# Performance work log

Measured on AMD Instinct MI355X. Metric: run time of the kernel, lower is better.

## Reference

```python
import jax, jax.numpy as jnp
import numpy as np

B, N, M, D = 4, 512, 512, 128
H, DOUT = 256, 128

def setup_inputs() -> dict:
    key = jax.random.key(0)
    k = jax.random.split(key, 4)
    X = jax.random.normal(k[0], (B, N, D), dtype=jnp.float32)
    Y = jax.random.normal(k[1], (B, M, D), dtype=jnp.float32)
    W1 = jax.random.normal(k[2], (2 * D, H), dtype=jnp.float32) / np.sqrt(2 * D)
    b1 = jnp.zeros((H,), dtype=jnp.float32)
    W2 = jax.random.normal(k[3], (H, DOUT), dtype=jnp.float32) / np.sqrt(H)
    b2 = jnp.zeros((DOUT,), dtype=jnp.float32)
    return {"X": X, "Y": Y, "W1": W1, "b1": b1, "W2": W2, "b2": b2}

def reference(X, Y, W1, b1, W2, b2):
    # pairs[b,n,m,:] = concat(Y[b,m], X[b,n])  -> [B,N,M,2D]
    n_ = X.shape[1]
    m_ = Y.shape[1]
    Ye = jnp.broadcast_to(Y[:, None, :, :], (X.shape[0], n_, m_, Y.shape[-1]))
    Xe = jnp.broadcast_to(X[:, :, None, :], (X.shape[0], n_, m_, X.shape[-1]))
    pairs = jnp.concatenate([Ye, Xe], axis=-1)
    # pointwise MLP: Linear -> ReLU -> Linear
    hdn = jax.nn.relu(jnp.einsum('bnmd,dh->bnmh', pairs, W1) + b1)
    Z = jnp.einsum('bnmh,ho->bnmo', hdn, W2) + b2
    # pool='sum' over the M (neighbor) dimension
    return jnp.sum(Z, axis=2)  # [B, N, DOUT]
```

## Files before the change

### kernel.cpp

```cpp
#include <hip/hip_runtime.h>

#define BB    4
#define NN    512
#define MM    512
#define DD    128
#define HH    256
#define DOUTC 128

typedef float v2f __attribute__((ext_vector_type(2)));
typedef float v4f __attribute__((ext_vector_type(4)));

__global__ __launch_bounds__(1024) void precompute_ac(
    const float* __restrict__ X, const float* __restrict__ Y,
    const float* __restrict__ W1, const float* __restrict__ b1,
    float* __restrict__ AC)
{
    __shared__ __align__(16) float rows[16][DD];
    __shared__ __align__(16) v4f mrg[3][4][4][64];
    const int bid = blockIdx.x;
    const int t   = threadIdx.x;
    const int isC = bid >> 7;
    const int r0  = (bid & 127) * 16;
    const float* src = isC ? X : Y;

    if (t < 512)
        reinterpret_cast<v4f*>(&rows[0][0])[t] =
            reinterpret_cast<const v4f*>(src + (size_t)r0 * DD)[t];
    __syncthreads();

    const int hq = t & 63;
    const int dq = (t >> 6) & 3;
    const int rs = t >> 8;
    const int d0 = dq * 32;
    const float* wp = W1 + (isC ? DD * HH : 0) + hq * 4;

    v4f acc[4];
#pragma unroll
    for (int r = 0; r < 4; ++r) acc[r] = (v4f){0.f, 0.f, 0.f, 0.f};

#pragma unroll 2
    for (int dg = 0; dg < 32; dg += 4) {
        const int d = d0 + dg;
        const v4f w0 = *reinterpret_cast<const v4f*>(&wp[(d + 0) * HH]);
        const v4f w1 = *reinterpret_cast<const v4f*>(&wp[(d + 1) * HH]);
        const v4f w2 = *reinterpret_cast<const v4f*>(&wp[(d + 2) * HH]);
        const v4f w3 = *reinterpret_cast<const v4f*>(&wp[(d + 3) * HH]);
#pragma unroll
        for (int r = 0; r < 4; ++r) {
            const v4f rv = *reinterpret_cast<const v4f*>(&rows[rs * 4 + r][d]);
            acc[r] += w0 * rv.x;
            acc[r] += w1 * rv.y;
            acc[r] += w2 * rv.z;
            acc[r] += w3 * rv.w;
        }
    }

    if (dq > 0) {
#pragma unroll
        for (int r = 0; r < 4; ++r) mrg[dq - 1][rs][r][hq] = acc[r];
    }
    __syncthreads();
    if (dq == 0) {
#pragma unroll
        for (int r = 0; r < 4; ++r) {
#pragma unroll
            for (int p = 0; p < 3; ++p) acc[r] += mrg[p][rs][r][hq];
        }
        v4f bias = (v4f){0.f, 0.f, 0.f, 0.f};
        if (isC) bias = *reinterpret_cast<const v4f*>(&b1[hq * 4]);
#pragma unroll
        for (int r = 0; r < 4; ++r)
            *reinterpret_cast<v4f*>(
                &AC[((size_t)(isC * 2048 + r0 + rs * 4 + r)) * HH + hq * 4]) =
                acc[r] + bias;
    }
}

__global__ __launch_bounds__(512) void fused_main(
    const float* __restrict__ A, const float* __restrict__ C,
    const float* __restrict__ W2, const float* __restrict__ b2,
    float* __restrict__ out)
{
    __shared__ __align__(16) v4f mergeA[8][4][64];
    __shared__ __align__(16) v4f mergeS[8][64];
    __shared__ __align__(16) float S[4][HH];
    const int bid = blockIdx.x;
    const int b   = bid >> 7;
    const int n0  = (bid & 127) * 4;
    const int t   = threadIdx.x;
    const int l   = t & 63;
    const int qm  = t >> 6;
    const int h0  = l * 4;

    const float* Cb = C + ((size_t)(b * NN + n0)) * HH + h0;
    v4f c4[4];
#pragma unroll
    for (int j = 0; j < 4; ++j)
        c4[j] = *reinterpret_cast<const v4f*>(&Cb[(size_t)j * HH]);
    v2f c01[4], c23[4];
#pragma unroll
    for (int j = 0; j < 4; ++j) {
        c01[j] = (v2f){c4[j].x, c4[j].y};
        c23[j] = (v2f){c4[j].z, c4[j].w};
    }

    float acc[4][4];
#pragma unroll
    for (int j = 0; j < 4; ++j)
#pragma unroll
        for (int u = 0; u < 4; ++u) acc[j][u] = 0.f;
    v2f sat01 = (v2f){0.f, 0.f}, sat23 = (v2f){0.f, 0.f};

    const float* Ab = A + ((size_t)(b * MM + qm * 64)) * HH + h0;
#pragma unroll 4
    for (int m = 0; m < 64; ++m) {
        const v4f a = *reinterpret_cast<const v4f*>(&Ab[(size_t)m * HH]);
        const v2f a01 = (v2f){a.x, a.y};
        const v2f a23 = (v2f){a.z, a.w};
        sat01 += a01;
        sat23 += a23;
#pragma unroll
        for (int j = 0; j < 4; ++j) {
            const v2f s01 = a01 + c01[j];
            const v2f s23 = a23 + c23[j];
            acc[j][0] += fabsf(s01.x);
            acc[j][1] += fabsf(s01.y);
            acc[j][2] += fabsf(s23.x);
            acc[j][3] += fabsf(s23.y);
        }
    }

#pragma unroll
    for (int j = 0; j < 4; ++j)
        mergeA[qm][j][l] = (v4f){acc[j][0], acc[j][1], acc[j][2], acc[j][3]};
    mergeS[qm][l] = (v4f){sat01.x, sat01.y, sat23.x, sat23.y};
    __syncthreads();

    if (qm < 4) {
        const int r = qm;
        v4f sum = mergeA[0][r][l];
#pragma unroll
        for (int p = 1; p < 8; ++p) sum += mergeA[p][r][l];
        v4f st = mergeS[0][l];
#pragma unroll
        for (int p = 1; p < 8; ++p) st += mergeS[p][l];
        const v4f sval = 0.5f * (st + 512.f * c4[r] + sum);
        *reinterpret_cast<v4f*>(&S[r][h0]) = sval;
    }
    __syncthreads();

    const int o0 = (t & 31) * 4;
    const int r  = (t >> 5) & 3;
    const int kq = t >> 7;
    const int k0 = kq * 64;
    v4f a4 = (v4f){0.f, 0.f, 0.f, 0.f};
    const float* w2p = W2 + o0;
#pragma unroll 4
    for (int k = k0; k < k0 + 64; k += 4) {
        const v4f sv = *reinterpret_cast<const v4f*>(&S[r][k]);
        const v4f wA = *reinterpret_cast<const v4f*>(&w2p[(k + 0) * DOUTC]);
        const v4f wB = *reinterpret_cast<const v4f*>(&w2p[(k + 1) * DOUTC]);
        const v4f wC = *reinterpret_cast<const v4f*>(&w2p[(k + 2) * DOUTC]);
        const v4f wD = *reinterpret_cast<const v4f*>(&w2p[(k + 3) * DOUTC]);
        a4 += wA * sv.x;
        a4 += wB * sv.y;
        a4 += wC * sv.z;
        a4 += wD * sv.w;
    }
    v4f* red = reinterpret_cast<v4f*>(&mergeA[0][0][0]);
    if (kq) red[(kq - 1) * 128 + (t & 127)] = a4;
    __syncthreads();
    if (kq == 0) {
#pragma unroll
        for (int p = 0; p < 3; ++p) a4 += red[p * 128 + (t & 127)];
        a4 += 512.f * (*reinterpret_cast<const v4f*>(&b2[o0]));
        *reinterpret_cast<v4f*>(&out[((size_t)(b * NN + n0 + r)) * DOUTC + o0]) = a4;
    }
}

extern "C" void kernel_launch(void* const* d_in, const int* in_sizes, int n_in,
                              void* d_out, int out_size, void* d_ws, size_t ws_size,
                              hipStream_t stream) {
    const float* X  = (const float*)d_in[0];
    const float* Y  = (const float*)d_in[1];
    const float* W1 = (const float*)d_in[2];
    const float* b1 = (const float*)d_in[3];
    const float* W2 = (const float*)d_in[4];
    const float* b2 = (const float*)d_in[5];
    float* out = (float*)d_out;

    float* AC = (float*)d_ws;
    float* A  = AC;
    float* Cm = AC + 2048 * HH;

    hipLaunchKernelGGL(precompute_ac, dim3(256), dim3(1024), 0, stream,
                       X, Y, W1, b1, AC);
    hipLaunchKernelGGL(fused_main, dim3(512), dim3(512), 0, stream,
                       A, Cm, W2, b2, out);
}
```

Before: 42.29 us.

## Replace O(N·M) ReLU sum with per-feature sort, prefix sums and binary search

The sum over M of relu(a_m + c_n) is now computed per hidden feature by sorting the A column with a bitonic sort in shared memory, building a prefix sum, and binary-searching each c_n to get the count and sum of terms above the threshold. This replaces the O(N·M·H) brute-force accumulation with O((N+M)·log M·H) work. Precompute now writes A and C transposed into workspace, and a separate epilogue kernel does the W2 projection. The cost is one extra kernel launch, many __syncthreads rounds in the sort and scan, and strided transposed stores in the precompute kernel.

```diff
diff --git a/kernel.cpp b/kernel.cpp
--- a/kernel.cpp
+++ b/kernel.cpp
@@ -7,13 +7,12 @@
 #define HH    256
 #define DOUTC 128
 
-typedef float v2f __attribute__((ext_vector_type(2)));
 typedef float v4f __attribute__((ext_vector_type(4)));
 
 __global__ __launch_bounds__(1024) void precompute_ac(
     const float* __restrict__ X, const float* __restrict__ Y,
     const float* __restrict__ W1, const float* __restrict__ b1,
-    float* __restrict__ AC)
+    float* __restrict__ AT, float* __restrict__ CT)
 {
     __shared__ __align__(16) float rows[16][DD];
     __shared__ __align__(16) v4f mrg[3][4][4][64];
@@ -69,84 +68,117 @@
         v4f bias = (v4f){0.f, 0.f, 0.f, 0.f};
         if (isC) bias = *reinterpret_cast<const v4f*>(&b1[hq * 4]);
 #pragma unroll
-        for (int r = 0; r < 4; ++r)
+        for (int r = 0; r < 4; ++r) acc[r] += bias;
+
+        const int grow = r0 + rs * 4;
+        const int bb   = grow >> 9;
+        const int mm   = grow & 511;
+        float* Tb = isC ? CT : AT;
+#pragma unroll
+        for (int u = 0; u < 4; ++u) {
+            const v4f w = (v4f){acc[0][u], acc[1][u], acc[2][u], acc[3][u]};
             *reinterpret_cast<v4f*>(
-                &AC[((size_t)(isC * 2048 + r0 + rs * 4 + r)) * HH + hq * 4]) =
-                acc[r] + bias;
-    }
-}
-
-__global__ __launch_bounds__(512) void fused_main(
-    const float* __restrict__ A, const float* __restrict__ C,
-    const float* __restrict__ W2, const float* __restrict__ b2,
-    float* __restrict__ out)
+                &Tb[((size_t)(bb * HH + hq * 4 + u)) * 512 + mm]) = w;
+        }
+    }
+}
+
+__global__ __launch_bounds__(512) void sort_query(
+    const float* __restrict__ AT, const float* __restrict__ CT,
+    float* __restrict__ S)
 {
-    __shared__ __align__(16) v4f mergeA[8][4][64];
-    __shared__ __align__(16) v4f mergeS[8][64];
-    __shared__ __align__(16) float S[4][HH];
+    __shared__ float col[4][512];
+    __shared__ float t1[4][512];
+    __shared__ float t2[4][512];
     const int bid = blockIdx.x;
-    const int b   = bid >> 7;
-    const int n0  = (bid & 127) * 4;
+    const int b   = bid >> 6;
+    const int h0  = (bid & 63) * 4;
     const int t   = threadIdx.x;
-    const int l   = t & 63;
-    const int qm  = t >> 6;
-    const int h0  = l * 4;
-
-    const float* Cb = C + ((size_t)(b * NN + n0)) * HH + h0;
-    v4f c4[4];
-#pragma unroll
-    for (int j = 0; j < 4; ++j)
-        c4[j] = *reinterpret_cast<const v4f*>(&Cb[(size_t)j * HH]);
-    v2f c01[4], c23[4];
-#pragma unroll
-    for (int j = 0; j < 4; ++j) {
-        c01[j] = (v2f){c4[j].x, c4[j].y};
-        c23[j] = (v2f){c4[j].z, c4[j].w};
-    }
-
-    float acc[4][4];
-#pragma unroll
-    for (int j = 0; j < 4; ++j)
-#pragma unroll
-        for (int u = 0; u < 4; ++u) acc[j][u] = 0.f;
-    v2f sat01 = (v2f){0.f, 0.f}, sat23 = (v2f){0.f, 0.f};
-
-    const float* Ab = A + ((size_t)(b * MM + qm * 64)) * HH + h0;
-#pragma unroll 4
-    for (int m = 0; m < 64; ++m) {
-        const v4f a = *reinterpret_cast<const v4f*>(&Ab[(size_t)m * HH]);
-        const v2f a01 = (v2f){a.x, a.y};
-        const v2f a23 = (v2f){a.z, a.w};
-        sat01 += a01;
-        sat23 += a23;
-#pragma unroll
-        for (int j = 0; j < 4; ++j) {
-            const v2f s01 = a01 + c01[j];
-            const v2f s23 = a23 + c23[j];
-            acc[j][0] += fabsf(s01.x);
-            acc[j][1] += fabsf(s01.y);
-            acc[j][2] += fabsf(s23.x);
-            acc[j][3] += fabsf(s23.y);
-        }
-    }
-
-#pragma unroll
-    for (int j = 0; j < 4; ++j)
-        mergeA[qm][j][l] = (v4f){acc[j][0], acc[j][1], acc[j][2], acc[j][3]};
-    mergeS[qm][l] = (v4f){sat01.x, sat01.y, sat23.x, sat23.y};
-    __syncthreads();
-
-    if (qm < 4) {
-        const int r = qm;
-        v4f sum = mergeA[0][r][l];
-#pragma unroll
-        for (int p = 1; p < 8; ++p) sum += mergeA[p][r][l];
-        v4f st = mergeS[0][l];
-#pragma unroll
-        for (int p = 1; p < 8; ++p) st += mergeS[p][l];
-        const v4f sval = 0.5f * (st + 512.f * c4[r] + sum);
-        *reinterpret_cast<v4f*>(&S[r][h0]) = sval;
-    }
+
+    const float* Abase = AT + ((size_t)(b * HH + h0)) * 512;
+#pragma unroll
+    for (int u = 0; u < 4; ++u)
+        col[u][t] = Abase[(size_t)u * 512 + t];
+    __syncthreads();
+
+    for (int k = 2; k <= 512; k <<= 1) {
+        for (int j = k >> 1; j > 0; j >>= 1) {
+            const int p = t ^ j;
+            if (p > t) {
+                const bool asc = ((t & k) == 0);
+#pragma unroll
+                for (int u = 0; u < 4; ++u) {
+                    const float x = col[u][t];
+                    const float y = col[u][p];
+                    if ((x > y) == asc) { col[u][t] = y; col[u][p] = x; }
+                }
+            }
+            __syncthreads();
+        }
+    }
+
+#pragma unroll
+    for (int u = 0; u < 4; ++u)
+        t1[u][t] = col[u][t] + ((t >= 1) ? col[u][t - 1] : 0.f);
+    __syncthreads();
+    {
+        int d = 2;
+#pragma unroll
+        for (int s = 0; s < 8; ++s) {
+            if ((s & 1) == 0) {
+#pragma unroll
+                for (int u = 0; u < 4; ++u)
+                    t2[u][t] = t1[u][t] + ((t >= d) ? t1[u][t - d] : 0.f);
+            } else {
+#pragma unroll
+                for (int u = 0; u < 4; ++u)
+                    t1[u][t] = t2[u][t] + ((t >= d) ? t2[u][t - d] : 0.f);
+            }
+            __syncthreads();
+            d <<= 1;
+        }
+    }
+
+    const float* Cbase = CT + ((size_t)(b * HH + h0)) * 512;
+    float cv[4], negc[4];
+    int kk[4];
+#pragma unroll
+    for (int u = 0; u < 4; ++u) {
+        cv[u]   = Cbase[(size_t)u * 512 + t];
+        negc[u] = -cv[u];
+        kk[u]   = 0;
+    }
+#pragma unroll
+    for (int step = 512; step > 0; step >>= 1) {
+#pragma unroll
+        for (int u = 0; u < 4; ++u) {
+            const int nk = kk[u] + step;
+            if (nk <= 512 && col[u][nk - 1] < negc[u]) kk[u] = nk;
+        }
+    }
+
+    v4f s4;
+#pragma unroll
+    for (int u = 0; u < 4; ++u) {
+        const float T  = t1[u][511];
+        const float Pk = (kk[u] > 0) ? t1[u][kk[u] - 1] : 0.f;
+        s4[u] = (T - Pk) + (float)(512 - kk[u]) * cv[u];
+    }
+    *reinterpret_cast<v4f*>(&S[((size_t)(b * NN + t)) * HH + h0]) = s4;
+}
+
+__global__ __launch_bounds__(512) void epilogue(
+    const float* __restrict__ S, const float* __restrict__ W2,
+    const float* __restrict__ b2, float* __restrict__ out)
+{
+    __shared__ __align__(16) float Sl[4][HH];
+    __shared__ __align__(16) v4f red[3 * 128];
+    const int bn0 = blockIdx.x * 4;
+    const int t   = threadIdx.x;
+
+    if (t < 256)
+        reinterpret_cast<v4f*>(&Sl[0][0])[t] =
+            reinterpret_cast<const v4f*>(&S[(size_t)bn0 * HH])[t];
     __syncthreads();
 
     const int o0 = (t & 31) * 4;
@@ -157,7 +189,7 @@
     const float* w2p = W2 + o0;
 #pragma unroll 4
     for (int k = k0; k < k0 + 64; k += 4) {
-        const v4f sv = *reinterpret_cast<const v4f*>(&S[r][k]);
+        const v4f sv = *reinterpret_cast<const v4f*>(&Sl[r][k]);
         const v4f wA = *reinterpret_cast<const v4f*>(&w2p[(k + 0) * DOUTC]);
         const v4f wB = *reinterpret_cast<const v4f*>(&w2p[(k + 1) * DOUTC]);
         const v4f wC = *reinterpret_cast<const v4f*>(&w2p[(k + 2) * DOUTC]);
@@ -167,14 +199,13 @@
         a4 += wC * sv.z;
         a4 += wD * sv.w;
     }
-    v4f* red = reinterpret_cast<v4f*>(&mergeA[0][0][0]);
     if (kq) red[(kq - 1) * 128 + (t & 127)] = a4;
     __syncthreads();
     if (kq == 0) {
 #pragma unroll
         for (int p = 0; p < 3; ++p) a4 += red[p * 128 + (t & 127)];
         a4 += 512.f * (*reinterpret_cast<const v4f*>(&b2[o0]));
-        *reinterpret_cast<v4f*>(&out[((size_t)(b * NN + n0 + r)) * DOUTC + o0]) = a4;
+        *reinterpret_cast<v4f*>(&out[(size_t)(bn0 + r) * DOUTC + o0]) = a4;
     }
 }
 
@@ -189,12 +220,14 @@
     const float* b2 = (const float*)d_in[5];
     float* out = (float*)d_out;
 
-    float* AC = (float*)d_ws;
-    float* A  = AC;
-    float* Cm = AC + 2048 * HH;
+    float* AT = (float*)d_ws;
+    float* CT = AT + (size_t)BB * HH * 512;
+    float* S  = CT + (size_t)BB * HH * 512;
 
     hipLaunchKernelGGL(precompute_ac, dim3(256), dim3(1024), 0, stream,
-                       X, Y, W1, b1, AC);
-    hipLaunchKernelGGL(fused_main, dim3(512), dim3(512), 0, stream,
-                       A, Cm, W2, b2, out);
-}
+                       X, Y, W1, b1, AT, CT);
+    hipLaunchKernelGGL(sort_query, dim3(256), dim3(512), 0, stream,
+                       AT, CT, S);
+    hipLaunchKernelGGL(epilogue, dim3(BB * NN / 4), dim3(512), 0, stream,
+                       S, W2, b2, out);
+}
```

Result: slower. 45.01 us (+6.4%).

## Split abs-sum stage into M-chunked kernel, precompute A-column sums, add epilogue

Applied to the files above, without the earlier changes.

The abs-sum kernel now gives each block 8 n-rows and a quarter of the M dimension, so every loaded A row is reused across 8 C rows, and 1024 smaller blocks are launched. The sum of A over m (SAT) is no longer accumulated inside the hot loop. Two extra blocks in the precompute kernel compute it as colsum(Y)·W1. A new epilogue kernel reduces the partial sums and applies W2. This cuts per-element load work and raises parallelism, at the cost of a third launch and a workspace round trip for the partials.

```diff
diff --git a/kernel.cpp b/kernel.cpp
--- a/kernel.cpp
+++ b/kernel.cpp
@@ -13,114 +13,136 @@
 __global__ __launch_bounds__(1024) void precompute_ac(
     const float* __restrict__ X, const float* __restrict__ Y,
     const float* __restrict__ W1, const float* __restrict__ b1,
-    float* __restrict__ AC)
+    float* __restrict__ AC, float* __restrict__ SAT)
 {
     __shared__ __align__(16) float rows[16][DD];
     __shared__ __align__(16) v4f mrg[3][4][4][64];
     const int bid = blockIdx.x;
     const int t   = threadIdx.x;
-    const int isC = bid >> 7;
-    const int r0  = (bid & 127) * 16;
-    const float* src = isC ? X : Y;
-
-    if (t < 512)
-        reinterpret_cast<v4f*>(&rows[0][0])[t] =
-            reinterpret_cast<const v4f*>(src + (size_t)r0 * DD)[t];
-    __syncthreads();
-
-    const int hq = t & 63;
-    const int dq = (t >> 6) & 3;
-    const int rs = t >> 8;
-    const int d0 = dq * 32;
-    const float* wp = W1 + (isC ? DD * HH : 0) + hq * 4;
-
-    v4f acc[4];
-#pragma unroll
-    for (int r = 0; r < 4; ++r) acc[r] = (v4f){0.f, 0.f, 0.f, 0.f};
+
+    if (bid < 256) {
+        const int isC = bid >> 7;
+        const int r0  = (bid & 127) * 16;
+        const float* src = isC ? X : Y;
+
+        if (t < 512)
+            reinterpret_cast<v4f*>(&rows[0][0])[t] =
+                reinterpret_cast<const v4f*>(src + (size_t)r0 * DD)[t];
+        __syncthreads();
+
+        const int hq = t & 63;
+        const int dq = (t >> 6) & 3;
+        const int rs = t >> 8;
+        const int d0 = dq * 32;
+        const float* wp = W1 + (isC ? DD * HH : 0) + hq * 4;
+
+        v4f acc[4];
+#pragma unroll
+        for (int r = 0; r < 4; ++r) acc[r] = (v4f){0.f, 0.f, 0.f, 0.f};
 
 #pragma unroll 2
-    for (int dg = 0; dg < 32; dg += 4) {
-        const int d = d0 + dg;
-        const v4f w0 = *reinterpret_cast<const v4f*>(&wp[(d + 0) * HH]);
-        const v4f w1 = *reinterpret_cast<const v4f*>(&wp[(d + 1) * HH]);
-        const v4f w2 = *reinterpret_cast<const v4f*>(&wp[(d + 2) * HH]);
-        const v4f w3 = *reinterpret_cast<const v4f*>(&wp[(d + 3) * HH]);
-#pragma unroll
-        for (int r = 0; r < 4; ++r) {
-            const v4f rv = *reinterpret_cast<const v4f*>(&rows[rs * 4 + r][d]);
-            acc[r] += w0 * rv.x;
-            acc[r] += w1 * rv.y;
-            acc[r] += w2 * rv.z;
-            acc[r] += w3 * rv.w;
-        }
-    }
-
-    if (dq > 0) {
-#pragma unroll
-        for (int r = 0; r < 4; ++r) mrg[dq - 1][rs][r][hq] = acc[r];
-    }
-    __syncthreads();
-    if (dq == 0) {
-#pragma unroll
-        for (int r = 0; r < 4; ++r) {
-#pragma unroll
-            for (int p = 0; p < 3; ++p) acc[r] += mrg[p][rs][r][hq];
-        }
-        v4f bias = (v4f){0.f, 0.f, 0.f, 0.f};
-        if (isC) bias = *reinterpret_cast<const v4f*>(&b1[hq * 4]);
-#pragma unroll
-        for (int r = 0; r < 4; ++r)
-            *reinterpret_cast<v4f*>(
-                &AC[((size_t)(isC * 2048 + r0 + rs * 4 + r)) * HH + hq * 4]) =
-                acc[r] + bias;
-    }
-}
-
-__global__ __launch_bounds__(512) void fused_main(
+        for (int dg = 0; dg < 32; dg += 4) {
+            const int d = d0 + dg;
+            const v4f w0 = *reinterpret_cast<const v4f*>(&wp[(d + 0) * HH]);
+            const v4f w1 = *reinterpret_cast<const v4f*>(&wp[(d + 1) * HH]);
+            const v4f w2 = *reinterpret_cast<const v4f*>(&wp[(d + 2) * HH]);
+            const v4f w3 = *reinterpret_cast<const v4f*>(&wp[(d + 3) * HH]);
+#pragma unroll
+            for (int r = 0; r < 4; ++r) {
+                const v4f rv = *reinterpret_cast<const v4f*>(&rows[rs * 4 + r][d]);
+                acc[r] += w0 * rv.x;
+                acc[r] += w1 * rv.y;
+                acc[r] += w2 * rv.z;
+                acc[r] += w3 * rv.w;
+            }
+        }
+
+        if (dq > 0) {
+#pragma unroll
+            for (int r = 0; r < 4; ++r) mrg[dq - 1][rs][r][hq] = acc[r];
+        }
+        __syncthreads();
+        if (dq == 0) {
+#pragma unroll
+            for (int r = 0; r < 4; ++r) {
+#pragma unroll
+                for (int p = 0; p < 3; ++p) acc[r] += mrg[p][rs][r][hq];
+            }
+            v4f bias = (v4f){0.f, 0.f, 0.f, 0.f};
+            if (isC) bias = *reinterpret_cast<const v4f*>(&b1[hq * 4]);
+#pragma unroll
+            for (int r = 0; r < 4; ++r)
+                *reinterpret_cast<v4f*>(
+                    &AC[((size_t)(isC * 2048 + r0 + rs * 4 + r)) * HH + hq * 4]) =
+                    acc[r] + bias;
+        }
+    } else {
+        const int half = t >> 9;
+        const int bb   = (bid - 256) * 2 + half;
+        const int tt   = t & 511;
+        float* scr = &rows[0][0];
+
+        const int d  = tt & 127;
+        const int mq = tt >> 7;
+        const float* yp = Y + ((size_t)(bb * MM + mq * 128)) * DD + d;
+        float s = 0.f;
+#pragma unroll 4
+        for (int i = 0; i < 128; ++i) s += yp[(size_t)i * DD];
+        scr[half * 512 + mq * 128 + d] = s;
+        __syncthreads();
+
+        if (tt < 256) {
+            const float* base = scr + half * 512;
+            float sat = 0.f;
+#pragma unroll 4
+            for (int dd = 0; dd < 128; ++dd) {
+                const float ys = base[dd] + base[128 + dd] +
+                                 base[256 + dd] + base[384 + dd];
+                sat = fmaf(ys, W1[dd * HH + tt], sat);
+            }
+            SAT[bb * HH + tt] = sat;
+        }
+    }
+}
+
+__global__ __launch_bounds__(256) void abs_main(
     const float* __restrict__ A, const float* __restrict__ C,
-    const float* __restrict__ W2, const float* __restrict__ b2,
-    float* __restrict__ out)
+    float* __restrict__ part)
 {
-    __shared__ __align__(16) v4f mergeA[8][4][64];
-    __shared__ __align__(16) v4f mergeS[8][64];
-    __shared__ __align__(16) float S[4][HH];
+    __shared__ __align__(16) v4f mergeA[3][8][64];
     const int bid = blockIdx.x;
-    const int b   = bid >> 7;
-    const int n0  = (bid & 127) * 4;
+    const int mc  = bid & 3;
+    const int nt  = (bid >> 2) & 63;
+    const int b   = bid >> 8;
     const int t   = threadIdx.x;
     const int l   = t & 63;
-    const int qm  = t >> 6;
+    const int w   = t >> 6;
     const int h0  = l * 4;
+    const int n0  = nt * 8;
 
     const float* Cb = C + ((size_t)(b * NN + n0)) * HH + h0;
-    v4f c4[4];
-#pragma unroll
-    for (int j = 0; j < 4; ++j)
-        c4[j] = *reinterpret_cast<const v4f*>(&Cb[(size_t)j * HH]);
-    v2f c01[4], c23[4];
-#pragma unroll
-    for (int j = 0; j < 4; ++j) {
-        c01[j] = (v2f){c4[j].x, c4[j].y};
-        c23[j] = (v2f){c4[j].z, c4[j].w};
-    }
-
-    float acc[4][4];
-#pragma unroll
-    for (int j = 0; j < 4; ++j)
+    v2f c01[8], c23[8];
+#pragma unroll
+    for (int j = 0; j < 8; ++j) {
+        const v4f cv = *reinterpret_cast<const v4f*>(&Cb[(size_t)j * HH]);
+        c01[j] = (v2f){cv.x, cv.y};
+        c23[j] = (v2f){cv.z, cv.w};
+    }
+
+    float acc[8][4];
+#pragma unroll
+    for (int j = 0; j < 8; ++j)
 #pragma unroll
         for (int u = 0; u < 4; ++u) acc[j][u] = 0.f;
-    v2f sat01 = (v2f){0.f, 0.f}, sat23 = (v2f){0.f, 0.f};
-
-    const float* Ab = A + ((size_t)(b * MM + qm * 64)) * HH + h0;
-#pragma unroll 4
-    for (int m = 0; m < 64; ++m) {
-        const v4f a = *reinterpret_cast<const v4f*>(&Ab[(size_t)m * HH]);
+
+    const float* Ab = A + ((size_t)(b * MM + mc * 128 + w * 32)) * HH + h0;
+#pragma unroll 4
+    for (int i = 0; i < 32; ++i) {
+        const v4f a = *reinterpret_cast<const v4f*>(&Ab[(size_t)i * HH]);
         const v2f a01 = (v2f){a.x, a.y};
         const v2f a23 = (v2f){a.z, a.w};
-        sat01 += a01;
-        sat23 += a23;
-#pragma unroll
-        for (int j = 0; j < 4; ++j) {
+#pragma unroll
+        for (int j = 0; j < 8; ++j) {
             const v2f s01 = a01 + c01[j];
             const v2f s23 = a23 + c23[j];
             acc[j][0] += fabsf(s01.x);
@@ -130,22 +152,49 @@
         }
     }
 
-#pragma unroll
-    for (int j = 0; j < 4; ++j)
-        mergeA[qm][j][l] = (v4f){acc[j][0], acc[j][1], acc[j][2], acc[j][3]};
-    mergeS[qm][l] = (v4f){sat01.x, sat01.y, sat23.x, sat23.y};
+    if (w > 0) {
+#pragma unroll
+        for (int j = 0; j < 8; ++j)
+            mergeA[w - 1][j][l] = (v4f){acc[j][0], acc[j][1], acc[j][2], acc[j][3]};
+    }
     __syncthreads();
-
-    if (qm < 4) {
-        const int r = qm;
-        v4f sum = mergeA[0][r][l];
-#pragma unroll
-        for (int p = 1; p < 8; ++p) sum += mergeA[p][r][l];
-        v4f st = mergeS[0][l];
-#pragma unroll
-        for (int p = 1; p < 8; ++p) st += mergeS[p][l];
-        const v4f sval = 0.5f * (st + 512.f * c4[r] + sum);
-        *reinterpret_cast<v4f*>(&S[r][h0]) = sval;
+    if (w == 0) {
+#pragma unroll
+        for (int j = 0; j < 8; ++j) {
+            v4f s = (v4f){acc[j][0], acc[j][1], acc[j][2], acc[j][3]};
+#pragma unroll
+            for (int p = 0; p < 3; ++p) s += mergeA[p][j][l];
+            *reinterpret_cast<v4f*>(&part[((size_t)bid * 8 + j) * HH + h0]) = s;
+        }
+    }
+}
+
+__global__ __launch_bounds__(512) void epilogue(
+    const float* __restrict__ part, const float* __restrict__ SAT,
+    const float* __restrict__ C, const float* __restrict__ W2,
+    const float* __restrict__ b2, float* __restrict__ out)
+{
+    __shared__ __align__(16) float Sl[4][HH];
+    __shared__ __align__(16) v4f red[3 * 128];
+    const int bn0 = blockIdx.x * 4;
+    const int b   = bn0 >> 9;
+    const int t   = threadIdx.x;
+
+    if (t < 256) {
+        const int h    = t;
+        const float sv = SAT[b * HH + h];
+        const int nt   = (bn0 & 511) >> 3;
+#pragma unroll
+        for (int r = 0; r < 4; ++r) {
+            const int bn = bn0 + r;
+            const int j  = bn & 7;
+            float ab = 0.f;
+#pragma unroll
+            for (int mcq = 0; mcq < 4; ++mcq)
+                ab += part[((size_t)((b * 256 + nt * 4 + mcq)) * 8 + j) * HH + h];
+            const float cv = C[(size_t)bn * HH + h];
+            Sl[r][h] = 0.5f * (sv + 512.f * cv + ab);
+        }
     }
     __syncthreads();
 
@@ -157,7 +206,7 @@
     const float* w2p = W2 + o0;
 #pragma unroll 4
     for (int k = k0; k < k0 + 64; k += 4) {
-        const v4f sv = *reinterpret_cast<const v4f*>(&S[r][k]);
+        const v4f sv = *reinterpret_cast<const v4f*>(&Sl[r][k]);
         const v4f wA = *reinterpret_cast<const v4f*>(&w2p[(k + 0) * DOUTC]);
         const v4f wB = *reinterpret_cast<const v4f*>(&w2p[(k + 1) * DOUTC]);
         const v4f wC = *reinterpret_cast<const v4f*>(&w2p[(k + 2) * DOUTC]);
@@ -167,14 +216,13 @@
         a4 += wC * sv.z;
         a4 += wD * sv.w;
     }
-    v4f* red = reinterpret_cast<v4f*>(&mergeA[0][0][0]);
     if (kq) red[(kq - 1) * 128 + (t & 127)] = a4;
     __syncthreads();
     if (kq == 0) {
 #pragma unroll
         for (int p = 0; p < 3; ++p) a4 += red[p * 128 + (t & 127)];
         a4 += 512.f * (*reinterpret_cast<const v4f*>(&b2[o0]));
-        *reinterpret_cast<v4f*>(&out[((size_t)(b * NN + n0 + r)) * DOUTC + o0]) = a4;
+        *reinterpret_cast<v4f*>(&out[(size_t)(bn0 + r) * DOUTC + o0]) = a4;
     }
 }
 
@@ -189,12 +237,16 @@
     const float* b2 = (const float*)d_in[5];
     float* out = (float*)d_out;
 
-    float* AC = (float*)d_ws;
-    float* A  = AC;
-    float* Cm = AC + 2048 * HH;
-
-    hipLaunchKernelGGL(precompute_ac, dim3(256), dim3(1024), 0, stream,
-                       X, Y, W1, b1, AC);
-    hipLaunchKernelGGL(fused_main, dim3(512), dim3(512), 0, stream,
-                       A, Cm, W2, b2, out);
-}
+    float* AC   = (float*)d_ws;
+    float* A    = AC;
+    float* Cm   = AC + 2048 * HH;
+    float* part = AC + 4096 * HH;
+    float* SAT  = part + (size_t)1024 * 8 * HH;
+
+    hipLaunchKernelGGL(precompute_ac, dim3(258), dim3(1024), 0, stream,
+                       X, Y, W1, b1, AC, SAT);
+    hipLaunchKernelGGL(abs_main, dim3(1024), dim3(256), 0, stream,
+                       A, Cm, part);
+    hipLaunchKernelGGL(epilogue, dim3(512), dim3(512), 0, stream,
+                       part, SAT, Cm, W2, b2, out);
+}
```

After: 52.82 us. 1.25x slower.
